# Kernel optimization log

Hardware: AMD Instinct MI355X
Metric: run time of the kernel (lower is better)

The kernel has to match this reference:

```python
import jax, jax.numpy as jnp
import numpy as np

DIM = 512; HEADS = 8; DH = 64; M = 256; ITERS = 6; N_PATCH = 10000; N_CLASSES = 2


def layernorm(x, w, b, eps=1e-5):
    mu = x.mean(-1, keepdims=True)
    var = ((x - mu) ** 2).mean(-1, keepdims=True)
    return (x - mu) * jax.lax.rsqrt(var + eps) * w + b


def pinv_iter(x, iters=ITERS):
    # Moore-Penrose iterative pseudo-inverse (lucidrains nystrom-attention)
    abs_x = jnp.abs(x)
    col = abs_x.sum(-1)
    row = abs_x.sum(-2)
    z = jnp.swapaxes(x, -1, -2) / (jnp.max(col) * jnp.max(row))
    I = jnp.eye(x.shape[-1], dtype=x.dtype)
    for _ in range(iters):
        xz = x @ z
        z = 0.25 * z @ (13 * I - xz @ (15 * I - xz @ (7 * I - xz)))
    return z


def nystrom_attn(x, qkv_w, out_w, out_b, res_w):
    b, n, _ = x.shape
    pad = (-n) % M  # front-pad so n divisible by num_landmarks
    xp = jnp.pad(x, ((0, 0), (pad, 0), (0, 0)))
    npad = n + pad
    qkv = (xp @ qkv_w).reshape(b, npad, 3, HEADS, DH)
    q = jnp.transpose(qkv[:, :, 0], (0, 2, 1, 3)) * (DH ** -0.5)  # [b,h,n,d]
    k = jnp.transpose(qkv[:, :, 1], (0, 2, 1, 3))
    v = jnp.transpose(qkv[:, :, 2], (0, 2, 1, 3))
    l = npad // M
    q_l = q.reshape(b, HEADS, M, l, DH).mean(3)  # landmark means [b,h,m,d]
    k_l = k.reshape(b, HEADS, M, l, DH).mean(3)
    attn1 = jax.nn.softmax(jnp.einsum('bhnd,bhmd->bhnm', q, k_l), -1)
    attn2 = jax.nn.softmax(jnp.einsum('bhid,bhjd->bhij', q_l, k_l), -1)
    attn3 = jax.nn.softmax(jnp.einsum('bhmd,bhnd->bhmn', q_l, k), -1)
    out = (attn1 @ pinv_iter(attn2)) @ (attn3 @ v)  # [b,h,n,d]
    pk = (res_w.shape[2] - 1) // 2
    out = out + jax.lax.conv_general_dilated(
        v, res_w, (1, 1), [(pk, pk), (0, 0)], feature_group_count=HEADS)
    out = jnp.transpose(out, (0, 2, 1, 3)).reshape(b, npad, HEADS * DH)
    out = out @ out_w + out_b
    return out[:, -n:]


def ppeg(x, H, W, w7, b7, w5, b5, w3, b3):
    B, _, C = x.shape
    cls_tok, feat = x[:, :1], x[:, 1:]
    f = jnp.transpose(feat, (0, 2, 1)).reshape(B, C, H, W)
    def dw(w, b):
        p = w.shape[2] // 2
        return jax.lax.conv_general_dilated(
            f, w, (1, 1), [(p, p), (p, p)], feature_group_count=C) + b[None, :, None, None]
    y = f + dw(w7, b7) + dw(w5, b5) + dw(w3, b3)
    y = jnp.transpose(y.reshape(B, C, H * W), (0, 2, 1))
    return jnp.concatenate([cls_tok, y], axis=1)


def setup_inputs() -> dict:
    key = jax.random.key(0)
    ks = jax.random.split(key, 16)
    d = {
        'x': jax.random.normal(ks[0], (1, N_PATCH, DIM), jnp.float32),
        'cls_token': jax.random.normal(ks[1], (1, 1, DIM), jnp.float32) * 1e-6,
        'ln1_w': jnp.ones((DIM,), jnp.float32), 'ln1_b': jnp.zeros((DIM,), jnp.float32),
        'qkv1_w': jax.random.normal(ks[2], (DIM, 3 * DIM), jnp.float32) * 0.03,
        'out1_w': jax.random.normal(ks[3], (DIM, DIM), jnp.float32) * 0.04,
        'out1_b': jnp.zeros((DIM,), jnp.float32),
        'res1_w': jax.random.normal(ks[4], (HEADS, 1, 33, 1), jnp.float32) * 0.1,
        'p7_w': jax.random.normal(ks[5], (DIM, 1, 7, 7), jnp.float32) * 0.1,
        'p7_b': jnp.zeros((DIM,), jnp.float32),
        'p5_w': jax.random.normal(ks[6], (DIM, 1, 5, 5), jnp.float32) * 0.1,
        'p5_b': jnp.zeros((DIM,), jnp.float32),
        'p3_w': jax.random.normal(ks[7], (DIM, 1, 3, 3), jnp.float32) * 0.1,
        'p3_b': jnp.zeros((DIM,), jnp.float32),
        'ln2_w': jnp.ones((DIM,), jnp.float32), 'ln2_b': jnp.zeros((DIM,), jnp.float32),
        'qkv2_w': jax.random.normal(ks[8], (DIM, 3 * DIM), jnp.float32) * 0.03,
        'out2_w': jax.random.normal(ks[9], (DIM, DIM), jnp.float32) * 0.04,
        'out2_b': jnp.zeros((DIM,), jnp.float32),
        'res2_w': jax.random.normal(ks[10], (HEADS, 1, 33, 1), jnp.float32) * 0.1,
        'norm_w': jnp.ones((DIM,), jnp.float32), 'norm_b': jnp.zeros((DIM,), jnp.float32),
        'fc2_w': jax.random.normal(ks[11], (DIM, N_CLASSES), jnp.float32) * 0.06,
        'fc2_b': jnp.zeros((N_CLASSES,), jnp.float32),
        'pc_w': jax.random.normal(ks[12], (DIM, N_CLASSES), jnp.float32) * 0.06,
        'pc_b': jnp.zeros((N_CLASSES,), jnp.float32),
    }
    return d


def reference(x, cls_token, ln1_w, ln1_b, qkv1_w, out1_w, out1_b, res1_w,
              p7_w, p7_b, p5_w, p5_b, p3_w, p3_b,
              ln2_w, ln2_b, qkv2_w, out2_w, out2_b, res2_w,
              norm_w, norm_b, fc2_w, fc2_b, pc_w, pc_b):
    h = x.astype(jnp.float32)
    B, n0, C = h.shape
    _H = int(np.ceil(np.sqrt(n0))); _W = _H
    add = _H * _W - n0
    if add > 0:
        h = jnp.concatenate([h, h[:, :add]], axis=1)
    h = jnp.concatenate([jnp.broadcast_to(cls_token, (B, 1, C)), h], axis=1)
    h = h + nystrom_attn(layernorm(h, ln1_w, ln1_b), qkv1_w, out1_w, out1_b, res1_w)
    h = ppeg(h, _H, _W, p7_w, p7_b, p5_w, p5_b, p3_w, p3_b)
    h = h + nystrom_attn(layernorm(h, ln2_w, ln2_b), qkv2_w, out2_w, out2_b, res2_w)
    hn = layernorm(h, norm_w, norm_b)
    cls_f = hn[:, 0]
    patch_f = hn[:, 1:]
    if add > 0:
        patch_f = patch_f[:, :n0]
    bag_logits = cls_f @ fc2_w + fc2_b
    patch_logits = patch_f @ pc_w + pc_b
    patch_scores = jax.nn.softmax(patch_logits, -1)
    return bag_logits, patch_logits, patch_scores
```

## Files before the change

### kernel.cpp

```cpp
#include <hip/hip_runtime.h>
#include <hip/hip_bf16.h>

#define DIM    512
#define HEADS  8
#define DHD    64
#define MLAND  256
#define NTOK   10001
#define NPATCH 10000
#define NPAD   10240
#define PADR   239
#define LFAC   40
#define MOUT   10112
#define NSPLIT 8

typedef __bf16 bf16x8_t __attribute__((ext_vector_type(8)));
typedef float  f32x4_t  __attribute__((ext_vector_type(4)));
typedef short  short8_t __attribute__((ext_vector_type(8)));

__device__ inline bf16x8_t bzero8() {
    union { short8_t s; bf16x8_t b; } u;
    u.s = (short8_t){0, 0, 0, 0, 0, 0, 0, 0};
    return u.b;
}

#define GLDS(gp, lp) __builtin_amdgcn_global_load_lds( \
    (const __attribute__((address_space(1))) void*)(gp), \
    (__attribute__((address_space(3))) void*)(lp), 16, 0, 0)

__global__ void k_concat(const float* __restrict__ x, const float* __restrict__ cls,
                         float* __restrict__ h) {
    int idx = blockIdx.x * 256 + threadIdx.x;
    if (idx >= NTOK * DIM) return;
    int row = idx / DIM, col = idx % DIM;
    h[idx] = (row == 0) ? cls[col] : x[(row - 1) * DIM + col];
}

__global__ __launch_bounds__(256) void k_layernorm_bf(
    const float* __restrict__ h, const float* __restrict__ w,
    const float* __restrict__ b, __hip_bfloat16* __restrict__ xbf) {
    int wave = threadIdx.x >> 6, lane = threadIdx.x & 63;
    int row = blockIdx.x * 4 + wave;
    if (row >= NTOK) return;
    const float* r = h + (long)row * DIM;
    int c0 = lane * 8;
    f32x4_t va = *(const f32x4_t*)(r + c0);
    f32x4_t vb = *(const f32x4_t*)(r + c0 + 4);
    float s = va[0] + va[1] + va[2] + va[3] + vb[0] + vb[1] + vb[2] + vb[3];
#pragma unroll
    for (int o = 32; o > 0; o >>= 1) s += __shfl_xor(s, o);
    float mu = s * (1.f / DIM);
    float d[8];
#pragma unroll
    for (int i = 0; i < 4; i++) { d[i] = va[i] - mu; d[4 + i] = vb[i] - mu; }
    float vs = 0.f;
#pragma unroll
    for (int i = 0; i < 8; i++) vs += d[i] * d[i];
#pragma unroll
    for (int o = 32; o > 0; o >>= 1) vs += __shfl_xor(vs, o);
    float rstd = rsqrtf(vs * (1.f / DIM) + 1e-5f);
    __hip_bfloat16 ob[8];
#pragma unroll
    for (int i = 0; i < 8; i++)
        ob[i] = __float2bfloat16(d[i] * rstd * w[c0 + i] + b[c0 + i]);
    *(uint4*)(xbf + (long)(PADR + row) * DIM + c0) = *(uint4*)ob;
}

__global__ void k_zerobf(__hip_bfloat16* __restrict__ p, int n) {
    int i = blockIdx.x * 256 + threadIdx.x;
    if (i < n) p[i] = __float2bfloat16(0.f);
}
__global__ void k_wt_cvt(const float* __restrict__ W, __hip_bfloat16* __restrict__ Wt,
                         int K, int N) {
    __shared__ float tile[32][33];
    int k0 = blockIdx.x * 32, n0 = blockIdx.y * 32;
    int lx = threadIdx.x % 32, ly = threadIdx.x / 32;
    for (int i = 0; i < 32; i += 8) tile[ly + i][lx] = W[(long)(k0 + ly + i) * N + n0 + lx];
    __syncthreads();
    for (int i = 0; i < 32; i += 8)
        Wt[(long)(n0 + ly + i) * K + k0 + lx] = __float2bfloat16(tile[lx][ly + i]);
}
__global__ void k_vt(const __hip_bfloat16* __restrict__ vh, __hip_bfloat16* __restrict__ vt) {
    __shared__ __hip_bfloat16 tile[32][33];
    int n0 = blockIdx.x * 32, d0 = blockIdx.y * 32, h = blockIdx.z;
    int lx = threadIdx.x % 32, ly = threadIdx.x / 32;
    for (int i = 0; i < 32; i += 8)
        tile[ly + i][lx] = vh[((long)h * NPAD + n0 + ly + i) * 64 + d0 + lx];
    __syncthreads();
    for (int i = 0; i < 32; i += 8)
        vt[((long)h * 64 + d0 + ly + i) * NPAD + n0 + lx] = tile[lx][ly + i];
}

__global__ __launch_bounds__(256) void k_qkv_gemm(
    const __hip_bfloat16* __restrict__ A, const __hip_bfloat16* __restrict__ Bt,
    __hip_bfloat16* __restrict__ qh, __hip_bfloat16* __restrict__ kh,
    __hip_bfloat16* __restrict__ vh)
{
    const int K = 512;
    __shared__ unsigned short As[2][128 * 64];
    __shared__ unsigned short Bs[2][128 * 64];
    int tid = threadIdx.x;
    int m0 = blockIdx.y * 128, n0 = blockIdx.x * 128;
    int wave = tid >> 6, lane = tid & 63;
    int wm = (wave & 1) * 64, wn = (wave >> 1) * 64;
    f32x4_t zero4 = {0.f, 0.f, 0.f, 0.f};
    f32x4_t acc[4][4];
#pragma unroll
    for (int i = 0; i < 4; i++)
#pragma unroll
        for (int j = 0; j < 4; j++) acc[i][j] = zero4;
    int quad = lane >> 4, fr = lane & 15;
    int lrow8 = lane >> 3, gls = lane & 7;
    int gg = gls ^ lrow8;

#define STAGE_AB(K0, AD, BD) do { \
    _Pragma("unroll") \
    for (int rnd = 0; rnd < 4; rnd++) { \
        int r0 = rnd * 32 + wave * 8; \
        int ar = r0 + lrow8; \
        GLDS(A  + (long)(m0 + ar) * K + (K0) + gg * 8, (AD) + r0 * 64); \
        GLDS(Bt + (long)(n0 + ar) * K + (K0) + gg * 8, (BD) + r0 * 64); \
    } \
} while (0)

    STAGE_AB(0, &As[0][0], &Bs[0][0]);
    for (int k0 = 0; k0 < K; k0 += 64) {
        int b = (k0 >> 6) & 1;
        if (k0 + 64 < K) {
            STAGE_AB(k0 + 64, &As[b ^ 1][0], &Bs[b ^ 1][0]);
            asm volatile("s_waitcnt vmcnt(8)" ::: "memory");
        } else {
            asm volatile("s_waitcnt vmcnt(0)" ::: "memory");
        }
        __builtin_amdgcn_s_barrier();
#pragma unroll
        for (int ks = 0; ks < 2; ks++) {
            int sg = (ks * 4 + quad) ^ (fr & 7);
            bf16x8_t af[4], bq[4];
#pragma unroll
            for (int i = 0; i < 4; i++) {
                af[i] = *(const bf16x8_t*)&As[b][(wm + i * 16 + fr) * 64 + sg * 8];
                bq[i] = *(const bf16x8_t*)&Bs[b][(wn + i * 16 + fr) * 64 + sg * 8];
            }
#pragma unroll
            for (int i = 0; i < 4; i++)
#pragma unroll
                for (int j = 0; j < 4; j++)
                    acc[i][j] = __builtin_amdgcn_mfma_f32_16x16x32_bf16(af[i], bq[j], acc[i][j], 0, 0, 0);
        }
        asm volatile("" ::: "memory");
        __builtin_amdgcn_s_barrier();
    }
#undef STAGE_AB
    int col = lane & 15, rq = lane >> 4;
#pragma unroll
    for (int j = 0; j < 4; j++) {
        int c = n0 + wn + j * 16 + col;
        int sect = c >> 9;
        int hh = (c >> 6) & 7;
        int d = c & 63;
        __hip_bfloat16* dst = (sect == 0) ? qh : (sect == 1) ? kh : vh;
        float sc = (sect == 0) ? 0.125f : 1.f;
#pragma unroll
        for (int i = 0; i < 4; i++) {
            int rbase = m0 + wm + i * 16 + rq * 4;
#pragma unroll
            for (int rr = 0; rr < 4; rr++) {
                int r = rbase + rr;
                dst[((long)hh * NPAD + r) * 64 + d] = __float2bfloat16(acc[i][j][rr] * sc);
            }
        }
    }
}

__global__ __launch_bounds__(256) void k_mfma_gemm(
    const __hip_bfloat16* __restrict__ A, const __hip_bfloat16* __restrict__ Bt,
    float* __restrict__ C, int M, int N, int K, int Mstore,
    const float* __restrict__ bias, int accum)
{
    __shared__ unsigned short As[2][128 * 64];
    __shared__ unsigned short Bs[2][128 * 64];
    int tid = threadIdx.x;
    int m0 = blockIdx.y * 128, n0 = blockIdx.x * 128;
    int wave = tid >> 6, lane = tid & 63;
    int wm = (wave & 1) * 64, wn = (wave >> 1) * 64;
    f32x4_t zero4 = {0.f, 0.f, 0.f, 0.f};
    f32x4_t acc[4][4];
#pragma unroll
    for (int i = 0; i < 4; i++)
#pragma unroll
        for (int j = 0; j < 4; j++) acc[i][j] = zero4;
    int quad = lane >> 4, fr = lane & 15;
    int lrow8 = lane >> 3, gls = lane & 7;
    int gg = gls ^ lrow8;

#define STAGE_AB(K0, AD, BD) do { \
    _Pragma("unroll") \
    for (int rnd = 0; rnd < 4; rnd++) { \
        int r0 = rnd * 32 + wave * 8; \
        int ar = r0 + lrow8; \
        GLDS(A  + (long)(m0 + ar) * K + (K0) + gg * 8, (AD) + r0 * 64); \
        GLDS(Bt + (long)(n0 + ar) * K + (K0) + gg * 8, (BD) + r0 * 64); \
    } \
} while (0)

    STAGE_AB(0, &As[0][0], &Bs[0][0]);
    for (int k0 = 0; k0 < K; k0 += 64) {
        int b = (k0 >> 6) & 1;
        if (k0 + 64 < K) {
            STAGE_AB(k0 + 64, &As[b ^ 1][0], &Bs[b ^ 1][0]);
            asm volatile("s_waitcnt vmcnt(8)" ::: "memory");
        } else {
            asm volatile("s_waitcnt vmcnt(0)" ::: "memory");
        }
        __builtin_amdgcn_s_barrier();
#pragma unroll
        for (int ks = 0; ks < 2; ks++) {
            int sg = (ks * 4 + quad) ^ (fr & 7);
            bf16x8_t af[4], bq[4];
#pragma unroll
            for (int i = 0; i < 4; i++) {
                af[i] = *(const bf16x8_t*)&As[b][(wm + i * 16 + fr) * 64 + sg * 8];
                bq[i] = *(const bf16x8_t*)&Bs[b][(wn + i * 16 + fr) * 64 + sg * 8];
            }
#pragma unroll
            for (int i = 0; i < 4; i++)
#pragma unroll
                for (int j = 0; j < 4; j++)
                    acc[i][j] = __builtin_amdgcn_mfma_f32_16x16x32_bf16(af[i], bq[j], acc[i][j], 0, 0, 0);
        }
        asm volatile("" ::: "memory");
        __builtin_amdgcn_s_barrier();
    }
#undef STAGE_AB
    int col = lane & 15, rq = lane >> 4;
#pragma unroll
    for (int j = 0; j < 4; j++) {
        int c = n0 + wn + j * 16 + col;
        float bsv = bias ? bias[c] : 0.f;
#pragma unroll
        for (int i = 0; i < 4; i++) {
            int rbase = m0 + wm + i * 16 + rq * 4;
#pragma unroll
            for (int rr = 0; rr < 4; rr++) {
                int r = rbase + rr;
                if (r >= Mstore) continue;
                float v = acc[i][j][rr] + bsv;
                long off = (long)r * N + c;
                if (accum) C[off] += v; else C[off] = v;
            }
        }
    }
}

__global__ __launch_bounds__(256) void k_mfma_t64(
    const __hip_bfloat16* __restrict__ A, long lda, long abatch, int arowmax,
    const __hip_bfloat16* __restrict__ Bt, long ldb, long bbatch,
    __hip_bfloat16* __restrict__ Cbf, long ldc, long cbatch, int ksplit)
{
    int h = blockIdx.z;
    const __hip_bfloat16* Ab = A + (long)h * abatch;
    const __hip_bfloat16* Bb = Bt + (long)h * bbatch;
    int m0 = blockIdx.y * 128;
    int kbeg = blockIdx.x * ksplit, kend = kbeg + ksplit;
    int wave = threadIdx.x >> 6, lane = threadIdx.x & 63;
    int wm = (wave & 1) * 64, wn = (wave >> 1) * 32;
    int fr = lane & 15, quad = lane >> 4;
    f32x4_t zero4 = {0.f, 0.f, 0.f, 0.f};
    f32x4_t acc[4][2];
#pragma unroll
    for (int i = 0; i < 4; i++) { acc[i][0] = zero4; acc[i][1] = zero4; }
    for (int k0 = kbeg; k0 < kend; k0 += 32) {
        bf16x8_t bq[2];
#pragma unroll
        for (int j = 0; j < 2; j++)
            bq[j] = *(const bf16x8_t*)(Bb + (long)(wn + j * 16 + fr) * ldb + k0 + quad * 8);
#pragma unroll
        for (int i = 0; i < 4; i++) {
            int r = m0 + wm + i * 16 + fr;
            bf16x8_t af = (r < arowmax) ? *(const bf16x8_t*)(Ab + (long)r * lda + k0 + quad * 8)
                                        : bzero8();
#pragma unroll
            for (int j = 0; j < 2; j++)
                acc[i][j] = __builtin_amdgcn_mfma_f32_16x16x32_bf16(af, bq[j], acc[i][j], 0, 0, 0);
        }
    }
#pragma unroll
    for (int i = 0; i < 4; i++)
#pragma unroll
        for (int j = 0; j < 2; j++)
#pragma unroll
            for (int rr = 0; rr < 4; rr++) {
                int r = m0 + wm + i * 16 + quad * 4 + rr;
                int c = wn + j * 16 + fr;
                Cbf[(long)h * cbatch + (long)c * ldc + r] = __float2bfloat16(acc[i][j][rr]);
            }
}

__global__ __launch_bounds__(256) void k_mm256(
    const __hip_bfloat16* __restrict__ Aa, const __hip_bfloat16* __restrict__ Bt,
    float s, float acoef, const __hip_bfloat16* __restrict__ Aadd,
    __hip_bfloat16* __restrict__ Ca, __hip_bfloat16* __restrict__ Ct)
{
    int hd = blockIdx.z;
    long hb = (long)hd * 65536;
    int m0 = blockIdx.y * 64, n0 = blockIdx.x * 32;
    int wave = threadIdx.x >> 6, lane = threadIdx.x & 63;
    int fr = lane & 15, quad = lane >> 4;
    int mrow = m0 + wave * 16;
    f32x4_t zero4 = {0.f, 0.f, 0.f, 0.f};
    f32x4_t acc[2];
    acc[0] = zero4; acc[1] = zero4;
#pragma unroll
    for (int k0 = 0; k0 < 256; k0 += 32) {
        bf16x8_t af = *(const bf16x8_t*)(Aa + hb + (long)(mrow + fr) * 256 + k0 + quad * 8);
#pragma unroll
        for (int j = 0; j < 2; j++) {
            bf16x8_t bq = *(const bf16x8_t*)(Bt + hb + (long)(n0 + j * 16 + fr) * 256 + k0 + quad * 8);
            acc[j] = __builtin_amdgcn_mfma_f32_16x16x32_bf16(af, bq, acc[j], 0, 0, 0);
        }
    }
#pragma unroll
    for (int j = 0; j < 2; j++)
#pragma unroll
        for (int rr = 0; rr < 4; rr++) {
            int r = mrow + quad * 4 + rr;
            int c = n0 + j * 16 + fr;
            float v = s * acc[j][rr];
            if (Aadd) v += acoef * __bfloat162float(Aadd[hb + (long)r * 256 + c]);
            __hip_bfloat16 bv = __float2bfloat16(v);
            if (Ca) Ca[hb + (long)r * 256 + c] = bv;
            if (Ct) Ct[hb + (long)c * 256 + r] = bv;
        }
}

__global__ __launch_bounds__(256) void k_pinvUW(
    const __hip_bfloat16* __restrict__ za, const __hip_bfloat16* __restrict__ xza,
    const __hip_bfloat16* __restrict__ xzt,
    __hip_bfloat16* __restrict__ ua, __hip_bfloat16* __restrict__ wt)
{
    int z = blockIdx.z;
    int hd = z & 7, isW = z >> 3;
    long hb = (long)hd * 65536;
    int m0 = blockIdx.y * 64, n0 = blockIdx.x * 32;
    int wave = threadIdx.x >> 6, lane = threadIdx.x & 63;
    int fr = lane & 15, quad = lane >> 4;
    int mrow = m0 + wave * 16;
    const __hip_bfloat16* Aa = isW ? xza : za;
    f32x4_t zero4 = {0.f, 0.f, 0.f, 0.f};
    f32x4_t acc[2];
    acc[0] = zero4; acc[1] = zero4;
#pragma unroll
    for (int k0 = 0; k0 < 256; k0 += 32) {
        bf16x8_t af = *(const bf16x8_t*)(Aa + hb + (long)(mrow + fr) * 256 + k0 + quad * 8);
#pragma unroll
        for (int j = 0; j < 2; j++) {
            bf16x8_t bq = *(const bf16x8_t*)(xzt + hb + (long)(n0 + j * 16 + fr) * 256 + k0 + quad * 8);
            acc[j] = __builtin_amdgcn_mfma_f32_16x16x32_bf16(af, bq, acc[j], 0, 0, 0);
        }
    }
#pragma unroll
    for (int j = 0; j < 2; j++)
#pragma unroll
        for (int rr = 0; rr < 4; rr++) {
            int r = mrow + quad * 4 + rr;
            int c = n0 + j * 16 + fr;
            __hip_bfloat16 bv = __float2bfloat16(acc[j][rr]);
            if (!isW) ua[hb + (long)r * 256 + c] = bv;
            else      wt[hb + (long)c * 256 + r] = bv;
        }
}

__global__ __launch_bounds__(256) void k_pinv3(
    const __hip_bfloat16* __restrict__ ua, const __hip_bfloat16* __restrict__ xzt,
    const __hip_bfloat16* __restrict__ wt, const __hip_bfloat16* __restrict__ za,
    __hip_bfloat16* __restrict__ Ca, __hip_bfloat16* __restrict__ Ct)
{
    int hd = blockIdx.z;
    long hb = (long)hd * 65536;
    int m0 = blockIdx.y * 64, n0 = blockIdx.x * 32;
    int wave = threadIdx.x >> 6, lane = threadIdx.x & 63;
    int fr = lane & 15, quad = lane >> 4;
    int mrow = m0 + wave * 16;
    f32x4_t zero4 = {0.f, 0.f, 0.f, 0.f};
    f32x4_t acc1[2], acc2[2];
    acc1[0] = zero4; acc1[1] = zero4; acc2[0] = zero4; acc2[1] = zero4;
#pragma unroll
    for (int k0 = 0; k0 < 256; k0 += 32) {
        bf16x8_t af = *(const bf16x8_t*)(ua + hb + (long)(mrow + fr) * 256 + k0 + quad * 8);
#pragma unroll
        for (int j = 0; j < 2; j++) {
            bf16x8_t b1 = *(const bf16x8_t*)(xzt + hb + (long)(n0 + j * 16 + fr) * 256 + k0 + quad * 8);
            bf16x8_t b2 = *(const bf16x8_t*)(wt  + hb + (long)(n0 + j * 16 + fr) * 256 + k0 + quad * 8);
            acc1[j] = __builtin_amdgcn_mfma_f32_16x16x32_bf16(af, b1, acc1[j], 0, 0, 0);
            acc2[j] = __builtin_amdgcn_mfma_f32_16x16x32_bf16(af, b2, acc2[j], 0, 0, 0);
        }
    }
#pragma unroll
    for (int j = 0; j < 2; j++)
#pragma unroll
        for (int rr = 0; rr < 4; rr++) {
            int r = mrow + quad * 4 + rr;
            int c = n0 + j * 16 + fr;
            float zv = __bfloat162float(za[hb + (long)r * 256 + c]);
            float uv = __bfloat162float(ua[hb + (long)r * 256 + c]);
            float v = 3.25f * zv - 3.75f * uv + 1.75f * acc1[j][rr] - 0.25f * acc2[j][rr];
            __hip_bfloat16 bv = __float2bfloat16(v);
            Ca[hb + (long)r * 256 + c] = bv;
            Ct[hb + (long)c * 256 + r] = bv;
        }
}

__global__ __launch_bounds__(256) void k_attn3f(
    const __hip_bfloat16* __restrict__ qlbf, const __hip_bfloat16* __restrict__ kh,
    const __hip_bfloat16* __restrict__ vt, float* __restrict__ part)
{
    int ns = blockIdx.x, mt = blockIdx.y, h = blockIdx.z;
    int wave = threadIdx.x >> 6, lane = threadIdx.x & 63;
    int fr = lane & 15, quad = lane >> 4;
    int lrow8 = lane >> 3, gls = lane & 7;
    int gg = gls ^ lrow8;
    int vsub = lane >> 5, vgrp = lane & 31;
    int swz = fr & 7;
    __shared__ unsigned short Ks[2][256 * 64];
    __shared__ unsigned short Vs[2][64 * 256];
    __shared__ __hip_bfloat16 Pl[64 * 136];
    f32x4_t zero4 = {0.f, 0.f, 0.f, 0.f};
    bf16x8_t aq[2];
    {
        const __hip_bfloat16* qb = qlbf + (long)h * 16384 + (long)(mt * 64 + wave * 16 + fr) * 64;
        aq[0] = *(const bf16x8_t*)(qb + quad * 8);
        aq[1] = *(const bf16x8_t*)(qb + 32 + quad * 8);
    }
    f32x4_t O[4];
#pragma unroll
    for (int j = 0; j < 4; j++) O[j] = zero4;
    float mr[4] = {-1e30f, -1e30f, -1e30f, -1e30f};
    float lr[4] = {0.f, 0.f, 0.f, 0.f};
    const __hip_bfloat16* kb = kh + (long)h * NPAD * 64;
    const __hip_bfloat16* vb = vt + (long)h * 64 * NPAD;

#define STAGE_KV(N0, KD, VD) do { \
    _Pragma("unroll") \
    for (int rnd = 0; rnd < 8; rnd++) { \
        int r0 = rnd * 32 + wave * 8; \
        GLDS(kb + (long)((N0) + r0 + lrow8) * 64 + gg * 8, (KD) + r0 * 64); \
    } \
    _Pragma("unroll") \
    for (int rnd = 0; rnd < 8; rnd++) { \
        int v0 = rnd * 8 + wave * 2; \
        int vrow = v0 + vsub; \
        GLDS(vb + (long)vrow * NPAD + (N0) + (vgrp ^ (vrow & 7)) * 8, (VD) + v0 * 256); \
    } \
} while (0)

    STAGE_KV(ns * 1280, &Ks[0][0], &Vs[0][0]);

    for (int nt = 0; nt < 5; nt++) {
        int bsel = nt & 1;
        if (nt < 4) {
            int n1 = ns * 1280 + (nt + 1) * 256;
            STAGE_KV(n1, &Ks[bsel ^ 1][0], &Vs[bsel ^ 1][0]);
            asm volatile("s_waitcnt vmcnt(16)" ::: "memory");
        } else {
            asm volatile("s_waitcnt vmcnt(0)" ::: "memory");
        }
        __builtin_amdgcn_s_barrier();

        const unsigned short* Kc = &Ks[bsel][0];
        const unsigned short* Vc = &Vs[bsel][0];
        f32x4_t s[16];
#pragma unroll
        for (int j = 0; j < 16; j++) s[j] = zero4;
#pragma unroll
        for (int j = 0; j < 16; j++) {
            const unsigned short* kr = Kc + (j * 16 + fr) * 64;
            bf16x8_t b0 = *(const bf16x8_t*)(kr + (quad ^ swz) * 8);
            bf16x8_t b1 = *(const bf16x8_t*)(kr + ((quad ^ swz) ^ 4) * 8);
            s[j] = __builtin_amdgcn_mfma_f32_16x16x32_bf16(aq[0], b0, s[j], 0, 0, 0);
            s[j] = __builtin_amdgcn_mfma_f32_16x16x32_bf16(aq[1], b1, s[j], 0, 0, 0);
        }
        float tm[4] = {-1e30f, -1e30f, -1e30f, -1e30f};
#pragma unroll
        for (int j = 0; j < 16; j++)
#pragma unroll
            for (int rr = 0; rr < 4; rr++) tm[rr] = fmaxf(tm[rr], s[j][rr]);
#pragma unroll
        for (int rr = 0; rr < 4; rr++) {
#pragma unroll
            for (int o = 8; o > 0; o >>= 1) tm[rr] = fmaxf(tm[rr], __shfl_xor(tm[rr], o));
        }
        float alpha[4], ts[4];
#pragma unroll
        for (int rr = 0; rr < 4; rr++) {
            float mnew = fmaxf(mr[rr], tm[rr]);
            alpha[rr] = __expf(mr[rr] - mnew);
            mr[rr] = mnew;
            ts[rr] = 0.f;
        }
#pragma unroll
        for (int j = 0; j < 16; j++)
#pragma unroll
            for (int rr = 0; rr < 4; rr++) {
                float e = __expf(s[j][rr] - mr[rr]);
                s[j][rr] = e;
                ts[rr] += e;
            }
#pragma unroll
        for (int rr = 0; rr < 4; rr++) {
#pragma unroll
            for (int o = 8; o > 0; o >>= 1) ts[rr] += __shfl_xor(ts[rr], o);
            lr[rr] = lr[rr] * alpha[rr] + ts[rr];
        }
#pragma unroll
        for (int j = 0; j < 4; j++)
#pragma unroll
            for (int rr = 0; rr < 4; rr++) O[j][rr] *= alpha[rr];
#pragma unroll
        for (int half = 0; half < 2; half++) {
#pragma unroll
            for (int j = 0; j < 8; j++)
#pragma unroll
                for (int rr = 0; rr < 4; rr++)
                    Pl[(wave * 16 + quad * 4 + rr) * 136 + j * 16 + fr] =
                        __float2bfloat16(s[half * 8 + j][rr]);
#pragma unroll
            for (int k0 = 0; k0 < 128; k0 += 32) {
                bf16x8_t af = *(const bf16x8_t*)&Pl[(wave * 16 + fr) * 136 + k0 + quad * 8];
                int gb = (half * 128 + k0) >> 3;
#pragma unroll
                for (int j = 0; j < 4; j++) {
                    const unsigned short* vr = Vc + (j * 16 + fr) * 256;
                    bf16x8_t bq = *(const bf16x8_t*)(vr + ((gb + quad) ^ swz) * 8);
                    O[j] = __builtin_amdgcn_mfma_f32_16x16x32_bf16(af, bq, O[j], 0, 0, 0);
                }
            }
        }
        asm volatile("" ::: "memory");
        __builtin_amdgcn_s_barrier();
    }
#undef STAGE_KV

    float* Ob = part + (long)((h * 4 + mt) * NSPLIT + ns) * 4224;
#pragma unroll
    for (int j = 0; j < 4; j++)
#pragma unroll
        for (int rr = 0; rr < 4; rr++)
            Ob[(wave * 16 + quad * 4 + rr) * 64 + j * 16 + fr] = O[j][rr];
    if (fr == 0) {
#pragma unroll
        for (int rr = 0; rr < 4; rr++) {
            Ob[4096 + wave * 16 + quad * 4 + rr] = mr[rr];
            Ob[4160 + wave * 16 + quad * 4 + rr] = lr[rr];
        }
    }
}

__global__ void k_a3comb(const float* __restrict__ part, __hip_bfloat16* __restrict__ a3vt) {
    int mt = blockIdx.x, h = blockIdx.y, t = threadIdx.x;
    int row = t >> 2, c0 = (t & 3) * 16;
    long base = (long)((h * 4 + mt) * NSPLIT) * 4224;
    float M = -1e30f;
    for (int s = 0; s < NSPLIT; s++) M = fmaxf(M, part[base + s * 4224 + 4096 + row]);
    float L = 0.f;
    float o[16];
#pragma unroll
    for (int c = 0; c < 16; c++) o[c] = 0.f;
    for (int s = 0; s < NSPLIT; s++) {
        const float* pb = part + base + (long)s * 4224;
        float w = __expf(pb[4096 + row] - M);
        L += pb[4160 + row] * w;
#pragma unroll
        for (int c = 0; c < 16; c++) o[c] += w * pb[row * 64 + c0 + c];
    }
    float invL = 1.f / L;
#pragma unroll
    for (int c = 0; c < 16; c++)
        a3vt[(long)h * 16384 + (long)(c0 + c) * 256 + mt * 64 + row] = __float2bfloat16(o[c] * invL);
}

__global__ void k_conv_res(const __hip_bfloat16* __restrict__ vh, const float* __restrict__ resw,
                           __hip_bfloat16* __restrict__ convbf) {
    int e4 = blockIdx.x * 256 + threadIdx.x;
    if (e4 >= NTOK * 128) return;
    int i = e4 >> 7;
    int c4 = (e4 & 127) * 4;
    int hh = c4 >> 6, d = c4 & 63;
    int n = PADR + i;
    const __hip_bfloat16* vb = vh + (long)hh * NPAD * 64 + d;
    float a0 = 0.f, a1 = 0.f, a2 = 0.f, a3 = 0.f;
#pragma unroll
    for (int t = 0; t < 33; t++) {
        int nn = n - 16 + t;
        if (nn < NPAD) {
            float w = resw[hh * 33 + t];
            uint2 pv = *(const uint2*)(vb + (long)nn * 64);
            __hip_bfloat16 vv[4];
            *(uint2*)vv = pv;
            a0 += w * __bfloat162float(vv[0]);
            a1 += w * __bfloat162float(vv[1]);
            a2 += w * __bfloat162float(vv[2]);
            a3 += w * __bfloat162float(vv[3]);
        }
    }
    __hip_bfloat16 o[4] = {__float2bfloat16(a0), __float2bfloat16(a1),
                           __float2bfloat16(a2), __float2bfloat16(a3)};
    *(uint2*)(convbf + (long)i * DIM + c4) = *(uint2*)o;
}

__global__ __launch_bounds__(256, 3) void k_attn1f(
    const __hip_bfloat16* __restrict__ qh, const __hip_bfloat16* __restrict__ klbf,
    const __hip_bfloat16* __restrict__ w2bt, const __hip_bfloat16* __restrict__ convbf,
    __hip_bfloat16* __restrict__ abf)
{
    int h = blockIdx.y;
    int i0 = blockIdx.x * 64;
    __shared__ __hip_bfloat16 Pl[64 * 136];
    __shared__ float mS[2][2][2][16];
    int tid = threadIdx.x;
    int wave = tid >> 6, lane = tid & 63;
    int rg = wave & 1, lh = wave >> 1;
    int fr = lane & 15, quad = lane >> 4;
    const __hip_bfloat16* kb = klbf + (long)h * (MLAND * DHD) + (long)lh * 128 * DHD;
    f32x4_t zero4 = {0.f, 0.f, 0.f, 0.f};

    f32x4_t s0[8], s1[8];
#pragma unroll
    for (int j = 0; j < 8; j++) { s0[j] = zero4; s1[j] = zero4; }
    int arow0 = i0 + rg * 16 + fr;
    int arow1 = arow0 + 32;
    const __hip_bfloat16* qrow = qh + ((long)h * NPAD + PADR + arow0) * 64;
#pragma unroll
    for (int k0 = 0; k0 < 64; k0 += 32) {
        bf16x8_t af0 = (arow0 < NTOK) ? *(const bf16x8_t*)(qrow + k0 + quad * 8) : bzero8();
        bf16x8_t af1 = (arow1 < NTOK) ? *(const bf16x8_t*)(qrow + 32 * 64 + k0 + quad * 8) : bzero8();
#pragma unroll
        for (int j = 0; j < 8; j++) {
            bf16x8_t bq = *(const bf16x8_t*)(kb + (long)(j * 16 + fr) * DHD + k0 + quad * 8);
            s0[j] = __builtin_amdgcn_mfma_f32_16x16x32_bf16(af0, bq, s0[j], 0, 0, 0);
            s1[j] = __builtin_amdgcn_mfma_f32_16x16x32_bf16(af1, bq, s1[j], 0, 0, 0);
        }
    }
    float sum0[4] = {0.f, 0.f, 0.f, 0.f}, sum1[4] = {0.f, 0.f, 0.f, 0.f};
#pragma unroll
    for (int j = 0; j < 8; j++)
#pragma unroll
        for (int rr = 0; rr < 4; rr++) {
            float e0 = __expf(s0[j][rr]); s0[j][rr] = e0; sum0[rr] += e0;
            float e1 = __expf(s1[j][rr]); s1[j][rr] = e1; sum1[rr] += e1;
        }
#pragma unroll
    for (int rr = 0; rr < 4; rr++) {
#pragma unroll
        for (int o = 8; o > 0; o >>= 1) {
            sum0[rr] += __shfl_xor(sum0[rr], o);
            sum1[rr] += __shfl_xor(sum1[rr], o);
        }
    }
    if (fr == 0) {
#pragma unroll
        for (int rr = 0; rr < 4; rr++) {
            mS[0][lh][rg][quad * 4 + rr] = sum0[rr];
            mS[1][lh][rg][quad * 4 + rr] = sum1[rr];
        }
    }
#pragma unroll
    for (int j = 0; j < 8; j++)
#pragma unroll
        for (int rr = 0; rr < 4; rr++) {
            Pl[(rg * 16 + quad * 4 + rr) * 136 + j * 16 + fr]      = __float2bfloat16(s0[j][rr]);
            Pl[(32 + rg * 16 + quad * 4 + rr) * 136 + j * 16 + fr] = __float2bfloat16(s1[j][rr]);
        }
    __syncthreads();
    float fac0[4], fac1[4];
#pragma unroll
    for (int rr = 0; rr < 4; rr++) {
        fac0[rr] = 1.f / (sum0[rr] + mS[0][lh ^ 1][rg][quad * 4 + rr]);
        fac1[rr] = 1.f / (sum1[rr] + mS[1][lh ^ 1][rg][quad * 4 + rr]);
    }
    float cp[2][4][4];
    if (lh == 0) {
#pragma unroll
        for (int rt = 0; rt < 2; rt++)
#pragma unroll
            for (int j = 0; j < 4; j++)
#pragma unroll
                for (int rr = 0; rr < 4; rr++) {
                    int r = i0 + rt * 32 + rg * 16 + quad * 4 + rr;
                    cp[rt][j][rr] = (r < NTOK)
                        ? __bfloat162float(convbf[(long)r * DIM + h * DHD + j * 16 + fr]) : 0.f;
                }
    }
    const __hip_bfloat16* wb = w2bt + (long)h * (DHD * MLAND) + lh * 128;
    f32x4_t oc0[4], oc1[4];
#pragma unroll
    for (int j = 0; j < 4; j++) { oc0[j] = zero4; oc1[j] = zero4; }
#pragma unroll
    for (int k0 = 0; k0 < 128; k0 += 32) {
        bf16x8_t af0 = *(const bf16x8_t*)&Pl[(rg * 16 + fr) * 136 + k0 + quad * 8];
        bf16x8_t af1 = *(const bf16x8_t*)&Pl[(32 + rg * 16 + fr) * 136 + k0 + quad * 8];
#pragma unroll
        for (int j = 0; j < 4; j++) {
            bf16x8_t bq = *(const bf16x8_t*)(wb + (long)(j * 16 + fr) * MLAND + k0 + quad * 8);
            oc0[j] = __builtin_amdgcn_mfma_f32_16x16x32_bf16(af0, bq, oc0[j], 0, 0, 0);
            oc1[j] = __builtin_amdgcn_mfma_f32_16x16x32_bf16(af1, bq, oc1[j], 0, 0, 0);
        }
    }
#pragma unroll
    for (int j = 0; j < 4; j++)
#pragma unroll
        for (int rr = 0; rr < 4; rr++) {
            oc0[j][rr] *= fac0[rr];
            oc1[j][rr] *= fac1[rr];
        }
    __syncthreads();
    float* ex = (float*)Pl;
    if (lh == 1) {
#pragma unroll
        for (int j = 0; j < 4; j++)
#pragma unroll
            for (int rr = 0; rr < 4; rr++) {
                ex[(rg * 16 + quad * 4 + rr) * 64 + j * 16 + fr]      = oc0[j][rr];
                ex[(32 + rg * 16 + quad * 4 + rr) * 64 + j * 16 + fr] = oc1[j][rr];
            }
    }
    __syncthreads();
    if (lh == 0) {
#pragma unroll
        for (int j = 0; j < 4; j++)
#pragma unroll
            for (int rr = 0; rr < 4; rr++) {
                int lr0 = rg * 16 + quad * 4 + rr;
                int r0 = i0 + lr0;
                if (r0 < NTOK) {
                    float v = oc0[j][rr] + ex[lr0 * 64 + j * 16 + fr] + cp[0][j][rr];
                    abf[(long)r0 * DIM + h * DHD + j * 16 + fr] = __float2bfloat16(v);
                }
                int r1 = r0 + 32;
                if (r1 < NTOK) {
                    float v = oc1[j][rr] + ex[(32 + lr0) * 64 + j * 16 + fr] + cp[1][j][rr];
                    abf[(long)r1 * DIM + h * DHD + j * 16 + fr] = __float2bfloat16(v);
                }
            }
    }
}

__global__ void k_landmarks(const __hip_bfloat16* __restrict__ qh,
                            const __hip_bfloat16* __restrict__ kh,
                            float* __restrict__ ql, float* __restrict__ kl,
                            __hip_bfloat16* __restrict__ qlbf, __hip_bfloat16* __restrict__ klbf) {
    int m = blockIdx.x, h = blockIdx.y, d = threadIdx.x;
    float sq = 0.f, sk = 0.f;
    for (int j = 0; j < LFAC; j++) {
        long base = ((long)h * NPAD + m * LFAC + j) * 64 + d;
        sq += __bfloat162float(qh[base]);
        sk += __bfloat162float(kh[base]);
    }
    long o = ((long)h * MLAND + m) * DHD + d;
    float vq = sq * (1.f / LFAC), vk = sk * (1.f / LFAC);
    ql[o] = vq; kl[o] = vk;
    qlbf[o] = __float2bfloat16(vq);
    klbf[o] = __float2bfloat16(vk);
}

__global__ void k_attn2(const float* __restrict__ ql, const float* __restrict__ kl,
                        float* __restrict__ attn2, __hip_bfloat16* __restrict__ attn2bf) {
    int i = blockIdx.x, h = blockIdx.y, j = threadIdx.x;
    __shared__ float q[64];
    __shared__ float red[256];
    if (j < 64) q[j] = ql[((long)h * MLAND + i) * DHD + j];
    __syncthreads();
    const float* kr = kl + ((long)h * MLAND + j) * DHD;
    float s = 0.f;
#pragma unroll 8
    for (int d = 0; d < 64; d++) s += q[d] * kr[d];
    red[j] = s; __syncthreads();
    for (int o = 128; o > 0; o >>= 1) { if (j < o) red[j] = fmaxf(red[j], red[j + o]); __syncthreads(); }
    float mx = red[0]; __syncthreads();
    float e = __expf(s - mx);
    red[j] = e; __syncthreads();
    for (int o = 128; o > 0; o >>= 1) { if (j < o) red[j] += red[j + o]; __syncthreads(); }
    float v = e / red[0];
    long off = ((long)h * MLAND + i) * MLAND + j;
    attn2[off] = v;
    attn2bf[off] = __float2bfloat16(v);
}

__global__ void k_colrow(const float* __restrict__ x, float* __restrict__ scal) {
    int h = blockIdx.x, t = threadIdx.x;
    const float* xh = x + (long)h * MLAND * MLAND;
    float rs = 0.f;
    for (int j = 0; j < MLAND; j++) rs += fabsf(xh[(long)j * MLAND + t]);
    __shared__ float red[256];
    red[t] = rs; __syncthreads();
    for (int o = 128; o > 0; o >>= 1) { if (t < o) red[t] = fmaxf(red[t], red[t + o]); __syncthreads(); }
    if (t == 0) { scal[10 + h] = red[0]; scal[2 + h] = 1.0f; }
}

__global__ void k_tscale2(const float* __restrict__ x, const float* __restrict__ scal,
                          __hip_bfloat16* __restrict__ za, __hip_bfloat16* __restrict__ zt) {
    int h = blockIdx.z;
    int tj = blockIdx.x * 32, ti = blockIdx.y * 32;
    __shared__ float tile[32][33];
    const float* xh = x + (long)h * 65536;
    int lx = threadIdx.x % 32, ly = threadIdx.x / 32;
    float cm = scal[2], rm = scal[10];
#pragma unroll
    for (int k = 1; k < 8; k++) {
        cm = fmaxf(cm, scal[2 + k]);
        rm = fmaxf(rm, scal[10 + k]);
    }
    float inv = 1.f / (cm * rm);
    for (int yy = 0; yy < 32; yy += 8) {
        float v = xh[(long)(ti + ly + yy) * MLAND + tj + lx];
        tile[ly + yy][lx] = v;
        zt[(long)h * 65536 + (long)(ti + ly + yy) * MLAND + tj + lx] = __float2bfloat16(v * inv);
    }
    __syncthreads();
    for (int yy = 0; yy < 32; yy += 8)
        za[(long)h * 65536 + (long)(tj + ly + yy) * MLAND + ti + lx] =
            __float2bfloat16(tile[lx][ly + yy] * inv);
}

__global__ void k_tfwd(const float* __restrict__ h, float* __restrict__ ft) {
    __shared__ float tile[32][33];
    int t0 = blockIdx.x * 32, c0 = blockIdx.y * 32;
    int lx = threadIdx.x % 32, ly = threadIdx.x / 32;
    for (int i = 0; i < 32; i += 8) {
        int t = t0 + ly + i;
        if (t < NPATCH) tile[ly + i][lx] = h[(long)(1 + t) * DIM + c0 + lx];
    }
    __syncthreads();
    for (int i = 0; i < 32; i += 8) {
        int c = c0 + ly + i, t = t0 + lx;
        if (t < NPATCH) ft[(long)c * NPATCH + t] = tile[lx][ly + i];
    }
}

__global__ __launch_bounds__(256) void k_ppeg2(
    const float* __restrict__ ft, float* __restrict__ yt,
    const float* __restrict__ w7, const float* __restrict__ b7,
    const float* __restrict__ w5, const float* __restrict__ b5,
    const float* __restrict__ w3, const float* __restrict__ b3)
{
    int s = blockIdx.x, c = blockIdx.y;
    __shared__ float tile[26][106];
    __shared__ float wt[49];
    int tid = threadIdx.x;
    int r0 = s * 20 - 3;
    for (int idx = tid; idx < 26 * 106; idx += 256) {
        int rr = idx / 106, cc = idx % 106;
        int gy = r0 + rr, gx = cc - 3;
        float v = 0.f;
        if (gy >= 0 && gy < 100 && gx >= 0 && gx < 100)
            v = ft[(long)c * NPATCH + gy * 100 + gx];
        tile[rr][cc] = v;
    }
    if (tid < 49) {
        int dy = tid / 7 - 3, dx = tid % 7 - 3;
        float w = w7[c * 49 + tid];
        if (dy >= -2 && dy <= 2 && dx >= -2 && dx <= 2) w += w5[c * 25 + (dy + 2) * 5 + (dx + 2)];
        if (dy >= -1 && dy <= 1 && dx >= -1 && dx <= 1) w += w3[c * 9 + (dy + 1) * 3 + (dx + 1)];
        wt[tid] = w;
    }
    __syncthreads();
    float bsum = b7[c] + b5[c] + b3[c];
    for (int p = tid; p < 2000; p += 256) {
        int ly = p / 100, lx = p % 100;
        float acc = tile[ly + 3][lx + 3] + bsum;
#pragma unroll
        for (int dy = 0; dy < 7; dy++)
#pragma unroll
            for (int dx = 0; dx < 7; dx++)
                acc += wt[dy * 7 + dx] * tile[ly + dy][lx + dx];
        yt[(long)c * NPATCH + (s * 20 + ly) * 100 + lx] = acc;
    }
}

__global__ void k_tback(const float* __restrict__ yt, float* __restrict__ h) {
    __shared__ float tile[32][33];
    int t0 = blockIdx.x * 32, c0 = blockIdx.y * 32;
    int lx = threadIdx.x % 32, ly = threadIdx.x / 32;
    for (int i = 0; i < 32; i += 8) {
        int c = c0 + ly + i, t = t0 + lx;
        if (t < NPATCH) tile[ly + i][lx] = yt[(long)c * NPATCH + t];
    }
    __syncthreads();
    for (int i = 0; i < 32; i += 8) {
        int t = t0 + ly + i;
        if (t < NPATCH) h[(long)(1 + t) * DIM + c0 + lx] = tile[lx][ly + i];
    }
}

__global__ __launch_bounds__(256) void k_final(
    const float* __restrict__ h, const float* __restrict__ nw,
    const float* __restrict__ nb,
    const float* __restrict__ fc2w, const float* __restrict__ fc2b,
    const float* __restrict__ pcw, const float* __restrict__ pcb,
    float* __restrict__ out)
{
    int wave = threadIdx.x >> 6, lane = threadIdx.x & 63;
    int row = blockIdx.x * 4 + wave;
    if (row >= NTOK) return;
    const float* r = h + (long)row * DIM;
    int c0 = lane * 8;
    f32x4_t va = *(const f32x4_t*)(r + c0);
    f32x4_t vb = *(const f32x4_t*)(r + c0 + 4);
    float s = va[0] + va[1] + va[2] + va[3] + vb[0] + vb[1] + vb[2] + vb[3];
#pragma unroll
    for (int o = 32; o > 0; o >>= 1) s += __shfl_xor(s, o);
    float mu = s * (1.f / DIM);
    float d[8];
#pragma unroll
    for (int i = 0; i < 4; i++) { d[i] = va[i] - mu; d[4 + i] = vb[i] - mu; }
    float vs = 0.f;
#pragma unroll
    for (int i = 0; i < 8; i++) vs += d[i] * d[i];
#pragma unroll
    for (int o = 32; o > 0; o >>= 1) vs += __shfl_xor(vs, o);
    float rstd = rsqrtf(vs * (1.f / DIM) + 1e-5f);
    const float* w = (row == 0) ? fc2w : pcw;
    float p0 = 0.f, p1 = 0.f;
#pragma unroll
    for (int i = 0; i < 8; i++) {
        float hn = d[i] * rstd * nw[c0 + i] + nb[c0 + i];
        p0 += hn * w[(c0 + i) * 2];
        p1 += hn * w[(c0 + i) * 2 + 1];
    }
#pragma unroll
    for (int o = 32; o > 0; o >>= 1) {
        p0 += __shfl_xor(p0, o);
        p1 += __shfl_xor(p1, o);
    }
    if (lane == 0) {
        const float* bb = (row == 0) ? fc2b : pcb;
        float a0 = p0 + bb[0], a1 = p1 + bb[1];
        if (row == 0) { out[0] = a0; out[1] = a1; }
        else {
            long i = row - 1;
            out[2 + i * 2] = a0;
            out[2 + i * 2 + 1] = a1;
            float m = fmaxf(a0, a1);
            float e0 = __expf(a0 - m), e1 = __expf(a1 - m);
            float inv = 1.f / (e0 + e1);
            out[2 + 2 * NPATCH + i * 2] = e0 * inv;
            out[2 + 2 * NPATCH + i * 2 + 1] = e1 * inv;
        }
    }
}

extern "C" void kernel_launch(void* const* d_in, const int* in_sizes, int n_in,
                              void* d_out, int out_size, void* d_ws, size_t ws_size,
                              hipStream_t stream)
{
    const float* x     = (const float*)d_in[0];
    const float* cls   = (const float*)d_in[1];
    const float* ln1w  = (const float*)d_in[2];
    const float* ln1b  = (const float*)d_in[3];
    const float* qkv1w = (const float*)d_in[4];
    const float* out1w = (const float*)d_in[5];
    const float* out1b = (const float*)d_in[6];
    const float* res1w = (const float*)d_in[7];
    const float* p7w   = (const float*)d_in[8];
    const float* p7b   = (const float*)d_in[9];
    const float* p5w   = (const float*)d_in[10];
    const float* p5b   = (const float*)d_in[11];
    const float* p3w   = (const float*)d_in[12];
    const float* p3b   = (const float*)d_in[13];
    const float* ln2w  = (const float*)d_in[14];
    const float* ln2b  = (const float*)d_in[15];
    const float* qkv2w = (const float*)d_in[16];
    const float* out2w = (const float*)d_in[17];
    const float* out2b = (const float*)d_in[18];
    const float* res2w = (const float*)d_in[19];
    const float* normw = (const float*)d_in[20];
    const float* normb = (const float*)d_in[21];
    const float* fc2w  = (const float*)d_in[22];
    const float* fc2b  = (const float*)d_in[23];
    const float* pcw   = (const float*)d_in[24];
    const float* pcb   = (const float*)d_in[25];
    float* out = (float*)d_out;

    float* p = (float*)d_ws;
    float* h      = p; p += 5120512;
    float* yt     = p; p += 5120512;
    float* ql     = p; p += 131072;
    float* kl     = p; p += 131072;
    float* x2     = p; p += 524288;
    float* scal   = p; p += 32;
    float* part   = p; p += 1081344;
    float* ft     = p; p += 5120512;
    __hip_bfloat16* qh     = (__hip_bfloat16*)p; p += 2621440;
    __hip_bfloat16* kh     = (__hip_bfloat16*)p; p += 2621440;
    __hip_bfloat16* vh     = (__hip_bfloat16*)p; p += 2621440;
    __hip_bfloat16* xbf    = (__hip_bfloat16*)p; p += 2621440;
    __hip_bfloat16* abf    = (__hip_bfloat16*)p; p += 2588672;
    __hip_bfloat16* convbf = (__hip_bfloat16*)p; p += 2560256;
    __hip_bfloat16* qw1t   = (__hip_bfloat16*)p; p += 393216;
    __hip_bfloat16* qw2t   = (__hip_bfloat16*)p; p += 393216;
    __hip_bfloat16* ow1t   = (__hip_bfloat16*)p; p += 131072;
    __hip_bfloat16* ow2t   = (__hip_bfloat16*)p; p += 131072;
    __hip_bfloat16* x2a    = (__hip_bfloat16*)p; p += 262144;
    __hip_bfloat16* za     = (__hip_bfloat16*)p; p += 262144;
    __hip_bfloat16* zt     = (__hip_bfloat16*)p; p += 262144;
    __hip_bfloat16* za2    = (__hip_bfloat16*)p; p += 262144;
    __hip_bfloat16* zt2    = (__hip_bfloat16*)p; p += 262144;
    __hip_bfloat16* xza    = (__hip_bfloat16*)p; p += 262144;
    __hip_bfloat16* xzt    = (__hip_bfloat16*)p; p += 262144;
    __hip_bfloat16* t1t    = (__hip_bfloat16*)p; p += 262144;
    __hip_bfloat16* t2t    = (__hip_bfloat16*)p; p += 262144;
    __hip_bfloat16* qlbf   = (__hip_bfloat16*)p; p += 65536;
    __hip_bfloat16* klbf   = (__hip_bfloat16*)p; p += 65536;
    __hip_bfloat16* vt     = (__hip_bfloat16*)p; p += 2621440;
    __hip_bfloat16* a3vt   = (__hip_bfloat16*)p; p += 65536;
    __hip_bfloat16* w2bt   = (__hip_bfloat16*)p; p += 65536;

    k_concat<<<dim3((NTOK * DIM + 255) / 256), 256, 0, stream>>>(x, cls, h);
    k_wt_cvt<<<dim3(16, 48), 256, 0, stream>>>(qkv1w, qw1t, 512, 1536);
    k_wt_cvt<<<dim3(16, 48), 256, 0, stream>>>(qkv2w, qw2t, 512, 1536);
    k_wt_cvt<<<dim3(16, 16), 256, 0, stream>>>(out1w, ow1t, 512, 512);
    k_wt_cvt<<<dim3(16, 16), 256, 0, stream>>>(out2w, ow2t, 512, 512);
    k_zerobf<<<dim3((PADR * DIM + 255) / 256), 256, 0, stream>>>(xbf, PADR * DIM);

    auto layer = [&](const float* lnw, const float* lnb, const __hip_bfloat16* qwt,
                     const __hip_bfloat16* owt, const float* outb, const float* resw) {
        k_layernorm_bf<<<dim3((NTOK + 3) / 4), 256, 0, stream>>>(h, lnw, lnb, xbf);
        k_qkv_gemm<<<dim3(12, 80), 256, 0, stream>>>(xbf, qwt, qh, kh, vh);
        k_vt<<<dim3(320, 2, HEADS), 256, 0, stream>>>(vh, vt);
        k_landmarks<<<dim3(MLAND, HEADS), 64, 0, stream>>>(qh, kh, ql, kl, qlbf, klbf);
        k_attn2<<<dim3(MLAND, HEADS), 256, 0, stream>>>(ql, kl, x2, x2a);
        k_colrow<<<HEADS, 256, 0, stream>>>(x2, scal);
        k_tscale2<<<dim3(8, 8, HEADS), 256, 0, stream>>>(x2, scal, za, zt);
        {
            __hip_bfloat16 *zra = za, *zrt = zt, *zoa = za2, *zot = zt2;
            dim3 g(8, 4, HEADS), g2(8, 4, 16);
            for (int it = 0; it < 6; it++) {
                k_mm256<<<g, 256, 0, stream>>>(x2a, zrt, 1.f, 0.f, nullptr, xza, xzt);
                k_pinvUW<<<g2, 256, 0, stream>>>(zra, xza, xzt, t1t, t2t);
                k_pinv3<<<g, 256, 0, stream>>>(t1t, xzt, t2t, zra, zoa, zot);
                __hip_bfloat16* tmp;
                tmp = zra; zra = zoa; zoa = tmp;
                tmp = zrt; zrt = zot; zot = tmp;
            }
        }
        k_attn3f<<<dim3(NSPLIT, 4, HEADS), 256, 0, stream>>>(qlbf, kh, vt, part);
        k_a3comb<<<dim3(4, HEADS), 256, 0, stream>>>(part, a3vt);
        k_mfma_t64<<<dim3(1, 2, HEADS), 256, 0, stream>>>(
            za, 256, 65536, 256, a3vt, 256, 16384,
            w2bt, 256, 16384, 256);
        k_conv_res<<<dim3((NTOK * 128 + 255) / 256), 256, 0, stream>>>(vh, resw, convbf);
        k_attn1f<<<dim3(157, HEADS), 256, 0, stream>>>(qh, klbf, w2bt, convbf, abf);
        k_mfma_gemm<<<dim3(4, 79), 256, 0, stream>>>(abf, owt, h, MOUT, 512, 512,
                                                     NTOK, outb, 1);
    };

    layer(ln1w, ln1b, qw1t, ow1t, out1b, res1w);

    k_tfwd<<<dim3(313, 16), 256, 0, stream>>>(h, ft);
    k_ppeg2<<<dim3(5, 512), 256, 0, stream>>>(ft, yt, p7w, p7b, p5w, p5b, p3w, p3b);
    k_tback<<<dim3(313, 16), 256, 0, stream>>>(yt, h);

    layer(ln2w, ln2b, qw2t, ow2t, out2b, res2w);

    k_final<<<dim3((NTOK + 3) / 4), 256, 0, stream>>>(h, normw, normb, fc2w, fc2b, pcw, pcb, out);
    (void)in_sizes; (void)n_in; (void)out_size; (void)ws_size;
}
```

Measured before the change: 877.8 us.

## Fuse V transpose into QKV GEMM epilogue, vectorize concat, balance attn output

```diff
diff --git a/kernel.cpp b/kernel.cpp
--- a/kernel.cpp
+++ b/kernel.cpp
@@ -29,10 +29,11 @@
 
 __global__ void k_concat(const float* __restrict__ x, const float* __restrict__ cls,
                          float* __restrict__ h) {
-    int idx = blockIdx.x * 256 + threadIdx.x;
-    if (idx >= NTOK * DIM) return;
-    int row = idx / DIM, col = idx % DIM;
-    h[idx] = (row == 0) ? cls[col] : x[(row - 1) * DIM + col];
+    int e = blockIdx.x * 256 + threadIdx.x;
+    if (e >= NTOK * 128) return;
+    int row = e >> 7, c4 = (e & 127) * 4;
+    const float* src = (row == 0) ? (cls + c4) : (x + (long)(row - 1) * DIM + c4);
+    *(f32x4_t*)(h + (long)row * DIM + c4) = *(const f32x4_t*)src;
 }
 
 __global__ __launch_bounds__(256) void k_layernorm_bf(
@@ -79,21 +80,11 @@
     for (int i = 0; i < 32; i += 8)
         Wt[(long)(n0 + ly + i) * K + k0 + lx] = __float2bfloat16(tile[lx][ly + i]);
 }
-__global__ void k_vt(const __hip_bfloat16* __restrict__ vh, __hip_bfloat16* __restrict__ vt) {
-    __shared__ __hip_bfloat16 tile[32][33];
-    int n0 = blockIdx.x * 32, d0 = blockIdx.y * 32, h = blockIdx.z;
-    int lx = threadIdx.x % 32, ly = threadIdx.x / 32;
-    for (int i = 0; i < 32; i += 8)
-        tile[ly + i][lx] = vh[((long)h * NPAD + n0 + ly + i) * 64 + d0 + lx];
-    __syncthreads();
-    for (int i = 0; i < 32; i += 8)
-        vt[((long)h * 64 + d0 + ly + i) * NPAD + n0 + lx] = tile[lx][ly + i];
-}
 
 __global__ __launch_bounds__(256) void k_qkv_gemm(
     const __hip_bfloat16* __restrict__ A, const __hip_bfloat16* __restrict__ Bt,
     __hip_bfloat16* __restrict__ qh, __hip_bfloat16* __restrict__ kh,
-    __hip_bfloat16* __restrict__ vh)
+    __hip_bfloat16* __restrict__ vh, __hip_bfloat16* __restrict__ vt)
 {
     const int K = 512;
     __shared__ unsigned short As[2][128 * 64];
@@ -168,6 +159,34 @@
                 int r = rbase + rr;
                 dst[((long)hh * NPAD + r) * 64 + d] = __float2bfloat16(acc[i][j][rr] * sc);
             }
+        }
+    }
+    if (n0 >= 1024) {
+        unsigned short* lt = &As[0][0];
+#pragma unroll
+        for (int j = 0; j < 4; j++) {
+            int cl = wn + j * 16 + col;
+            int sw = (cl & 15) << 3;
+#pragma unroll
+            for (int i = 0; i < 4; i++)
+#pragma unroll
+                for (int rr = 0; rr < 4; rr++) {
+                    int rl = wm + i * 16 + rq * 4 + rr;
+                    __hip_bfloat16 bv = __float2bfloat16(acc[i][j][rr]);
+                    lt[cl * 128 + (rl ^ sw)] = *(unsigned short*)&bv;
+                }
+        }
+        __syncthreads();
+        int cr = tid >> 1, half = tid & 1;
+        int cg = n0 + cr;
+        int dd = cg & 63, hh2 = (cg >> 6) & 7;
+        int sw = (cr & 15) << 3;
+        __hip_bfloat16* dstv = vt + ((long)hh2 * 64 + dd) * NPAD + m0;
+#pragma unroll
+        for (int k = 0; k < 8; k++) {
+            int R = half * 64 + k * 8;
+            uint4 v = *(uint4*)&lt[cr * 128 + (R ^ sw)];
+            *(uint4*)(dstv + R) = v;
         }
     }
 }
@@ -677,19 +696,6 @@
         fac0[rr] = 1.f / (sum0[rr] + mS[0][lh ^ 1][rg][quad * 4 + rr]);
         fac1[rr] = 1.f / (sum1[rr] + mS[1][lh ^ 1][rg][quad * 4 + rr]);
     }
-    float cp[2][4][4];
-    if (lh == 0) {
-#pragma unroll
-        for (int rt = 0; rt < 2; rt++)
-#pragma unroll
-            for (int j = 0; j < 4; j++)
-#pragma unroll
-                for (int rr = 0; rr < 4; rr++) {
-                    int r = i0 + rt * 32 + rg * 16 + quad * 4 + rr;
-                    cp[rt][j][rr] = (r < NTOK)
-                        ? __bfloat162float(convbf[(long)r * DIM + h * DHD + j * 16 + fr]) : 0.f;
-                }
-    }
     const __hip_bfloat16* wb = w2bt + (long)h * (DHD * MLAND) + lh * 128;
     f32x4_t oc0[4], oc1[4];
 #pragma unroll
@@ -712,36 +718,43 @@
             oc0[j][rr] *= fac0[rr];
             oc1[j][rr] *= fac1[rr];
         }
+    float cp[4][4];
+#pragma unroll
+    for (int j = 0; j < 4; j++)
+#pragma unroll
+        for (int rr = 0; rr < 4; rr++) {
+            int r = i0 + lh * 32 + rg * 16 + quad * 4 + rr;
+            cp[j][rr] = (r < NTOK)
+                ? __bfloat162float(convbf[(long)r * DIM + h * DHD + j * 16 + fr]) : 0.f;
+        }
     __syncthreads();
     float* ex = (float*)Pl;
     if (lh == 1) {
 #pragma unroll
         for (int j = 0; j < 4; j++)
 #pragma unroll
-            for (int rr = 0; rr < 4; rr++) {
-                ex[(rg * 16 + quad * 4 + rr) * 64 + j * 16 + fr]      = oc0[j][rr];
+            for (int rr = 0; rr < 4; rr++)
+                ex[(rg * 16 + quad * 4 + rr) * 64 + j * 16 + fr] = oc0[j][rr];
+    } else {
+#pragma unroll
+        for (int j = 0; j < 4; j++)
+#pragma unroll
+            for (int rr = 0; rr < 4; rr++)
                 ex[(32 + rg * 16 + quad * 4 + rr) * 64 + j * 16 + fr] = oc1[j][rr];
+    }
+    __syncthreads();
+    f32x4_t* ocm = lh ? oc1 : oc0;
+#pragma unroll
+    for (int j = 0; j < 4; j++)
+#pragma unroll
+        for (int rr = 0; rr < 4; rr++) {
+            int lr0 = lh * 32 + rg * 16 + quad * 4 + rr;
+            int r = i0 + lr0;
+            if (r < NTOK) {
+                float v = ocm[j][rr] + ex[lr0 * 64 + j * 16 + fr] + cp[j][rr];
+                abf[(long)r * DIM + h * DHD + j * 16 + fr] = __float2bfloat16(v);
             }
-    }
-    __syncthreads();
-    if (lh == 0) {
-#pragma unroll
-        for (int j = 0; j < 4; j++)
-#pragma unroll
-            for (int rr = 0; rr < 4; rr++) {
-                int lr0 = rg * 16 + quad * 4 + rr;
-                int r0 = i0 + lr0;
-                if (r0 < NTOK) {
-                    float v = oc0[j][rr] + ex[lr0 * 64 + j * 16 + fr] + cp[0][j][rr];
-                    abf[(long)r0 * DIM + h * DHD + j * 16 + fr] = __float2bfloat16(v);
-                }
-                int r1 = r0 + 32;
-                if (r1 < NTOK) {
-                    float v = oc1[j][rr] + ex[(32 + lr0) * 64 + j * 16 + fr] + cp[1][j][rr];
-                    abf[(long)r1 * DIM + h * DHD + j * 16 + fr] = __float2bfloat16(v);
-                }
-            }
-    }
+        }
 }
 
 __global__ void k_landmarks(const __hip_bfloat16* __restrict__ qh,
@@ -1014,7 +1027,7 @@
     __hip_bfloat16* a3vt   = (__hip_bfloat16*)p; p += 65536;
     __hip_bfloat16* w2bt   = (__hip_bfloat16*)p; p += 65536;
 
-    k_concat<<<dim3((NTOK * DIM + 255) / 256), 256, 0, stream>>>(x, cls, h);
+    k_concat<<<dim3((NTOK * 128 + 255) / 256), 256, 0, stream>>>(x, cls, h);
     k_wt_cvt<<<dim3(16, 48), 256, 0, stream>>>(qkv1w, qw1t, 512, 1536);
     k_wt_cvt<<<dim3(16, 48), 256, 0, stream>>>(qkv2w, qw2t, 512, 1536);
     k_wt_cvt<<<dim3(16, 16), 256, 0, stream>>>(out1w, ow1t, 512, 512);
@@ -1024,8 +1037,7 @@
     auto layer = [&](const float* lnw, const float* lnb, const __hip_bfloat16* qwt,
                      const __hip_bfloat16* owt, const float* outb, const float* resw) {
         k_layernorm_bf<<<dim3((NTOK + 3) / 4), 256, 0, stream>>>(h, lnw, lnb, xbf);
-        k_qkv_gemm<<<dim3(12, 80), 256, 0, stream>>>(xbf, qwt, qh, kh, vh);
-        k_vt<<<dim3(320, 2, HEADS), 256, 0, stream>>>(vh, vt);
+        k_qkv_gemm<<<dim3(12, 80), 256, 0, stream>>>(xbf, qwt, qh, kh, vh, vt);
         k_landmarks<<<dim3(MLAND, HEADS), 64, 0, stream>>>(qh, kh, ql, kl, qlbf, klbf);
         k_attn2<<<dim3(MLAND, HEADS), 256, 0, stream>>>(ql, kl, x2, x2a);
         k_colrow<<<HEADS, 256, 0, stream>>>(x2, scal);
```

Result: no change. 869.1 us (-1.0%).
